# Optimization experiments

Hardware: AMD Instinct MI355X
Metric: run time of the kernel (lower is better)

Reference implementation:

```python
import jax, jax.numpy as jnp
import numpy as np

V, E = 50000, 800000
NODE_IN, EDGE_IN, OUT, HEADS = 128, 16, 32, 4
NEG_SLOPE = 0.2  # DGL EdgeGATConv default negative_slope


def setup_inputs() -> dict:
    key = jax.random.key(0)
    ks = jax.random.split(key, 10)
    return {
        "node_feats": jax.random.normal(ks[0], (V, NODE_IN), jnp.float32),
        "edge_feats": jax.random.normal(ks[1], (E, EDGE_IN), jnp.float32),
        "src": jax.random.randint(ks[2], (E,), 0, V),
        "dst": jax.random.randint(ks[3], (E,), 0, V),
        "W_node": jax.random.normal(ks[4], (NODE_IN, HEADS * OUT), jnp.float32) * 0.05,
        "W_edge": jax.random.normal(ks[5], (EDGE_IN, HEADS * OUT), jnp.float32) * 0.05,
        "attn_l": jax.random.normal(ks[6], (HEADS, OUT), jnp.float32) * 0.05,
        "attn_r": jax.random.normal(ks[7], (HEADS, OUT), jnp.float32) * 0.05,
        "attn_e": jax.random.normal(ks[8], (HEADS, OUT), jnp.float32) * 0.05,
        "res_W": jax.random.normal(ks[9], (NODE_IN, HEADS * OUT), jnp.float32) * 0.05,
        "bias": jnp.zeros((HEADS * OUT,), jnp.float32),
    }


def _leaky_relu(x, slope):
    return jnp.where(x >= 0, x, slope * x)


def reference(node_feats, edge_feats, src, dst, W_node, W_edge, attn_l, attn_r, attn_e, res_W, bias):
    V = node_feats.shape[0]
    H, F = attn_l.shape
    # linear projections
    ft = (node_feats @ W_node).reshape(V, H, F)    # [V,H,F]
    fe = (edge_feats @ W_edge).reshape(-1, H, F)   # [E,H,F]
    # per-head attention logits
    el = jnp.einsum('vhf,hf->vh', ft, attn_l)      # [V,H]
    er = jnp.einsum('vhf,hf->vh', ft, attn_r)      # [V,H]
    ee = jnp.einsum('ehf,hf->eh', fe, attn_e)      # [E,H]
    e = _leaky_relu(el[src] + er[dst] + ee, NEG_SLOPE)  # [E,H]
    # edge softmax over incoming edges of each destination node (stable)
    emax = jax.ops.segment_max(e, dst, num_segments=V)  # [V,H]
    ex = jnp.exp(e - emax[dst])
    esum = jax.ops.segment_sum(ex, dst, num_segments=V)  # [V,H]
    a = ex / esum[dst]                                   # [E,H]
    # weighted message passing: u_mul_e(ft, a) then sum to dst
    msg = ft[src] * a[:, :, None]                        # [E,H,F]
    rst = jax.ops.segment_sum(msg, dst, num_segments=V)  # [V,H,F]
    # residual connection + bias (EdgeGATConv residual=True, bias=True)
    rst = rst + (node_feats @ res_W).reshape(V, H, F)
    rst = rst + bias.reshape(1, H, F)
    # agg_mode='flatten': concat heads
    return rst.reshape(V, H * F)
```

## Files before the change

### kernel.cpp

```cpp
#include <hip/hip_runtime.h>
#include <hip/hip_fp16.h>
#include <cstdint>

#define V_N 50000
#define E_N 800000
#define NODE_IN 128
#define EDGE_IN 16
#define HF 128
#define NEG_SLOPE 0.2f
#define NB_SCAN 196
#define NODE_BLKS 1563
#define HIST_BLKS 3125

#define OFF_FT    0
#define OFF_EL    3200000
#define OFF_ER    3400000
#define OFF_DEG   3600000
#define OFF_ROW   3650000
#define OFF_BSUM  3700004
#define OFF_RANK  3700260
#define OFF_REC   4500260
#define OFF_WATT  7700260
#define OFF_BFRAG 7700324

typedef short bf16x8 __attribute__((ext_vector_type(8)));
typedef float f32x4 __attribute__((ext_vector_type(4)));

__device__ __forceinline__ unsigned short f2bf(float f) {
    unsigned u = __float_as_uint(f);
    u += 0x7fffu + ((u >> 16) & 1u);
    return (unsigned short)(u >> 16);
}
__device__ __forceinline__ unsigned pk2(float lo, float hi) {
    return (unsigned)f2bf(lo) | ((unsigned)f2bf(hi) << 16);
}
__device__ __forceinline__ float bflo(unsigned w) { return __uint_as_float(w << 16); }
__device__ __forceinline__ float bfhi(unsigned w) { return __uint_as_float(w & 0xffff0000u); }

typedef __fp16 fp16x2 __attribute__((ext_vector_type(2)));
__device__ __forceinline__ unsigned pkh2(float a, float b) {
    fp16x2 h = __builtin_amdgcn_cvt_pkrtz(a, b);
    return __builtin_bit_cast(unsigned, h);
}
__device__ __forceinline__ __half2 u2h(unsigned u) {
    return __builtin_bit_cast(__half2, u);
}
__device__ __forceinline__ unsigned h2u(__half2 h) {
    return __builtin_bit_cast(unsigned, h);
}

__global__ void k_prep(const float* __restrict__ We,
                       const float* __restrict__ attn_e,
                       const float* __restrict__ Wn,
                       const float* __restrict__ Wr,
                       float* __restrict__ watt,
                       unsigned* __restrict__ bfrag,
                       int* __restrict__ deg) {
    int g = blockIdx.x * 256 + threadIdx.x;
    for (int i = g; i < V_N; i += 16384) deg[i] = 0;
    if (blockIdx.x == 0 && threadIdx.x < 64) {
        int k = threadIdx.x >> 2, h = threadIdx.x & 3;
        float s = 0.f;
        #pragma unroll
        for (int f = 0; f < 32; f++)
            s += We[k * HF + h * 32 + f] * attn_e[h * 32 + f];
        watt[k * 4 + h] = s;
    }
    if (g < 16384) {
        int c    = g >> 8;
        int lane = (g >> 2) & 63;
        int jp   = g & 3;
        int nt = c >> 2, ks = c & 3;
        int col = nt * 16 + (lane & 15);
        int k   = ks * 32 + (lane >> 4) * 8 + jp * 2;
        const float* W = (col < 128) ? Wn : Wr;
        int cc = col & 127;
        float x0 = W[(size_t)k * 128 + cc];
        float x1 = W[(size_t)(k + 1) * 128 + cc];
        bfrag[g] = pk2(x0, x1);
    }
}

__global__ __launch_bounds__(256) void k_nodehist(
    const float* __restrict__ nf, const unsigned* __restrict__ bfragw,
    const float* __restrict__ attn_l, const float* __restrict__ attn_r,
    const float* __restrict__ bias, const int* __restrict__ dst,
    unsigned* __restrict__ ftw, float* __restrict__ el,
    float* __restrict__ er, float* __restrict__ out,
    int* __restrict__ deg, int* __restrict__ rank)
{
    __shared__ __align__(16) float sSf[32 * 140];
    unsigned short* sA = (unsigned short*)sSf;

    if (blockIdx.x >= NODE_BLKS) {
        int e = (blockIdx.x - NODE_BLKS) * 256 + threadIdx.x;
        rank[e] = atomicAdd(&deg[dst[e]], 1);
        return;
    }

    const int t = threadIdx.x;
    const int lane = t & 63;
    const int w = t >> 6;
    const int nb = blockIdx.x * 32;
    const int n15 = lane & 15;
    const int q = lane >> 4;
    const unsigned short* bfrag = (const unsigned short*)bfragw;

    #pragma unroll
    for (int i = 0; i < 4; i++) {
        int f = t + i * 256;
        int node = f >> 5;
        int kc = (f & 31) * 4;
        float4 v = {0.f, 0.f, 0.f, 0.f};
        if (nb + node < V_N)
            v = *(const float4*)(nf + (size_t)(nb + node) * NODE_IN + kc);
        uint2 u2 = make_uint2(pk2(v.x, v.y), pk2(v.z, v.w));
        *(uint2*)&sA[node * 136 + kc] = u2;
    }
    __syncthreads();

    f32x4 acc[2][4];
    #pragma unroll
    for (int m = 0; m < 2; m++)
        #pragma unroll
        for (int tt = 0; tt < 4; tt++) acc[m][tt] = (f32x4){0.f, 0.f, 0.f, 0.f};

    #pragma unroll
    for (int ks = 0; ks < 4; ks++) {
        bf16x8 a0 = *(const bf16x8*)&sA[n15 * 136 + ks * 32 + q * 8];
        bf16x8 a1 = *(const bf16x8*)&sA[(16 + n15) * 136 + ks * 32 + q * 8];
        #pragma unroll
        for (int tt = 0; tt < 4; tt++) {
            int nt = (tt < 2) ? (2 * w + tt) : (8 + 2 * w + (tt - 2));
            bf16x8 b = *(const bf16x8*)(bfrag + ((size_t)(nt * 4 + ks) * 64 + lane) * 8);
            acc[0][tt] = __builtin_amdgcn_mfma_f32_16x16x32_bf16(a0, b, acc[0][tt], 0, 0, 0);
            acc[1][tt] = __builtin_amdgcn_mfma_f32_16x16x32_bf16(a1, b, acc[1][tt], 0, 0, 0);
        }
    }

    {
        float al0 = attn_l[w * 32 + n15];
        float al1 = attn_l[w * 32 + 16 + n15];
        float ar0 = attn_r[w * 32 + n15];
        float ar1 = attn_r[w * 32 + 16 + n15];
        #pragma unroll
        for (int m = 0; m < 2; m++) {
            #pragma unroll
            for (int r = 0; r < 4; r++) {
                float fa = acc[m][0][r], fb = acc[m][1][r];
                float elp = fa * al0 + fb * al1;
                float erp = fa * ar0 + fb * ar1;
                elp += __shfl_xor(elp, 1); erp += __shfl_xor(erp, 1);
                elp += __shfl_xor(elp, 2); erp += __shfl_xor(erp, 2);
                elp += __shfl_xor(elp, 4); erp += __shfl_xor(erp, 4);
                elp += __shfl_xor(elp, 8); erp += __shfl_xor(erp, 8);
                int node = nb + m * 16 + q * 4 + r;
                if (n15 == 0 && node < V_N) {
                    el[node * 4 + w] = elp;
                    er[node * 4 + w] = erp;
                }
            }
        }
    }
    #pragma unroll
    for (int m = 0; m < 2; m++)
        #pragma unroll
        for (int r = 0; r < 4; r++) {
            int node = nb + m * 16 + q * 4 + r;
            if (node < V_N)
                ftw[(size_t)node * 64 + w * 16 + n15] =
                    pkh2(acc[m][0][r], acc[m][1][r]);
        }
    __syncthreads();

    #pragma unroll
    for (int m = 0; m < 2; m++)
        #pragma unroll
        for (int tt = 2; tt < 4; tt++)
            #pragma unroll
            for (int r = 0; r < 4; r++)
                sSf[(m * 16 + q * 4 + r) * 140 + w * 32 + (tt - 2) * 16 + n15] =
                    acc[m][tt][r];
    __syncthreads();
    #pragma unroll
    for (int i = 0; i < 4; i++) {
        int u = t + i * 256;
        int node = u >> 5, c4 = (u & 31) * 4;
        if (nb + node < V_N) {
            float4 v = *(float4*)&sSf[node * 140 + c4];
            float4 b4 = *(const float4*)(bias + c4);
            v.x += b4.x; v.y += b4.y; v.z += b4.z; v.w += b4.w;
            *(float4*)(out + (size_t)(nb + node) * HF + c4) = v;
        }
    }
}

__global__ __launch_bounds__(256) void k_scan(const int* __restrict__ deg,
                                              int* __restrict__ rowp) {
    __shared__ int sh[256];
    int t = threadIdx.x, b = blockIdx.x;

    int pre = 0;
    for (int i = t; i < b * 256; i += 256) pre += deg[i];
    sh[t] = pre;
    __syncthreads();
    #pragma unroll
    for (int off = 128; off > 0; off >>= 1) {
        if (t < off) sh[t] += sh[t + off];
        __syncthreads();
    }
    int sbase = sh[0];
    __syncthreads();

    int i = b * 256 + t;
    int v = (i < V_N) ? deg[i] : 0;
    sh[t] = v;
    __syncthreads();
    #pragma unroll
    for (int off = 1; off < 256; off <<= 1) {
        int u = (t >= off) ? sh[t - off] : 0;
        __syncthreads();
        sh[t] += u;
        __syncthreads();
    }
    if (i < V_N) rowp[i] = sbase + sh[t] - v;
    if (i == 0) rowp[V_N] = E_N;
}

__global__ __launch_bounds__(256) void k_escatter(
    const float* __restrict__ ef, const int* __restrict__ src,
    const int* __restrict__ dst, const int* __restrict__ rank,
    const int* __restrict__ rowp, const float* __restrict__ watt,
    const float* __restrict__ el, uint4* __restrict__ rec)
{
    __shared__ float sw[64];
    __shared__ __align__(16) float see[256][4];
    const int t = threadIdx.x;
    if (t < 64) sw[t] = watt[t];
    __syncthreads();
    const int base = blockIdx.x * 256;
    const int lane = t & 63, w = t >> 6;
    const int k0 = (lane & 3) * 4;

    #pragma unroll
    for (int r = 0; r < 4; r++) {
        int le = w * 64 + r * 16 + (lane >> 2);
        float4 v = *(const float4*)(ef + (size_t)(base + le) * EDGE_IN + k0);
        float e0 = 0.f, e1 = 0.f, e2 = 0.f, e3 = 0.f;
        float vv[4] = {v.x, v.y, v.z, v.w};
        #pragma unroll
        for (int j = 0; j < 4; j++) {
            int k = k0 + j;
            e0 += vv[j] * sw[k * 4 + 0];
            e1 += vv[j] * sw[k * 4 + 1];
            e2 += vv[j] * sw[k * 4 + 2];
            e3 += vv[j] * sw[k * 4 + 3];
        }
        e0 += __shfl_xor(e0, 1); e1 += __shfl_xor(e1, 1);
        e2 += __shfl_xor(e2, 1); e3 += __shfl_xor(e3, 1);
        e0 += __shfl_xor(e0, 2); e1 += __shfl_xor(e1, 2);
        e2 += __shfl_xor(e2, 2); e3 += __shfl_xor(e3, 2);
        if ((lane & 3) == 0) {
            float4 o = {e0, e1, e2, e3};
            *(float4*)&see[le][0] = o;
        }
    }
    __syncthreads();

    int e = base + t;
    int s = src[e], d = dst[e];
    int p = rowp[d] + rank[e];
    float4 ee = *(float4*)&see[t][0];
    float4 el4 = *(const float4*)(el + (size_t)s * 4);
    uint4 rr;
    rr.x = (unsigned)s;
    rr.y = pk2(el4.x + ee.x, el4.y + ee.y);
    rr.z = pk2(el4.z + ee.z, el4.w + ee.w);
    rr.w = 0;
    rec[p] = rr;
}

__global__ __launch_bounds__(256) void k_gather(
    const int* __restrict__ row, const uint4* __restrict__ rec,
    const float* __restrict__ er,
    const unsigned* __restrict__ ftw, float* __restrict__ out)
{
    __shared__ unsigned aw[4][64][4];
    const int lane = threadIdx.x & 63;
    const int wid  = threadIdx.x >> 6;
    const int d = blockIdx.x * 4 + wid;
    if (d >= V_N) return;
    const int n0 = row[d];
    const int deg = row[d + 1] - n0;
    if (deg == 0) return;

    const float4 er4 = *(const float4*)(er + (size_t)d * 4);

    const int qw = lane >> 4, li = lane & 15;
    const int head = li >> 2;
    float4 s4 = {0.f, 0.f, 0.f, 0.f};
    __half2 ha0 = u2h(0u), ha1 = u2h(0u), ha2 = u2h(0u), ha3 = u2h(0u);
    __half2 hb0 = u2h(0u), hb1 = u2h(0u), hb2 = u2h(0u), hb3 = u2h(0u);

    for (int i0 = 0; i0 < deg; i0 += 64) {
        int chunk = min(64, deg - i0);
        int si = 0;
        float4 ex = {0.f, 0.f, 0.f, 0.f};
        if (lane < chunk) {
            uint4 r = rec[n0 + i0 + lane];
            si = (int)r.x;
            float x0 = bflo(r.y) + er4.x;
            float x1 = bfhi(r.y) + er4.y;
            float x2 = bflo(r.z) + er4.z;
            float x3 = bfhi(r.z) + er4.w;
            x0 = x0 >= 0.f ? x0 : NEG_SLOPE * x0;
            x1 = x1 >= 0.f ? x1 : NEG_SLOPE * x1;
            x2 = x2 >= 0.f ? x2 : NEG_SLOPE * x2;
            x3 = x3 >= 0.f ? x3 : NEG_SLOPE * x3;
            ex.x = __expf(x0); ex.y = __expf(x1);
            ex.z = __expf(x2); ex.w = __expf(x3);
            s4.x += ex.x; s4.y += ex.y; s4.z += ex.z; s4.w += ex.w;
        }
        uint4 ap;
        ap.x = pkh2(ex.x, ex.x); ap.y = pkh2(ex.y, ex.y);
        ap.z = pkh2(ex.z, ex.z); ap.w = pkh2(ex.w, ex.w);
        *(uint4*)&aw[wid][lane][0] = ap;
        asm volatile("s_waitcnt lgkmcnt(0)" ::: "memory");

        int iters = (chunk + 7) & ~7;
        for (int j = 0; j < iters; j += 8) {
            int jq0 = j + qw, jq1 = j + qw + 4;
            int sidx0 = __shfl(si, jq0);
            int sidx1 = __shfl(si, jq1);
            unsigned au0 = aw[wid][jq0][head];
            unsigned au1 = aw[wid][jq1][head];
            uint4 wv0 = *(const uint4*)(ftw + (size_t)sidx0 * 64 + li * 4);
            uint4 wv1 = *(const uint4*)(ftw + (size_t)sidx1 * 64 + li * 4);
            ha0 = __hfma2(u2h(wv0.x), u2h(au0), ha0);
            ha1 = __hfma2(u2h(wv0.y), u2h(au0), ha1);
            ha2 = __hfma2(u2h(wv0.z), u2h(au0), ha2);
            ha3 = __hfma2(u2h(wv0.w), u2h(au0), ha3);
            hb0 = __hfma2(u2h(wv1.x), u2h(au1), hb0);
            hb1 = __hfma2(u2h(wv1.y), u2h(au1), hb1);
            hb2 = __hfma2(u2h(wv1.z), u2h(au1), hb2);
            hb3 = __hfma2(u2h(wv1.w), u2h(au1), hb3);
        }
    }
    #pragma unroll
    for (int off = 1; off < 64; off <<= 1) {
        s4.x += __shfl_xor(s4.x, off);
        s4.y += __shfl_xor(s4.y, off);
        s4.z += __shfl_xor(s4.z, off);
        s4.w += __shfl_xor(s4.w, off);
    }
    ha0 = __hadd2(ha0, hb0); ha1 = __hadd2(ha1, hb1);
    ha2 = __hadd2(ha2, hb2); ha3 = __hadd2(ha3, hb3);
    ha0 = __hadd2(ha0, u2h(__shfl_xor(h2u(ha0), 16)));
    ha1 = __hadd2(ha1, u2h(__shfl_xor(h2u(ha1), 16)));
    ha2 = __hadd2(ha2, u2h(__shfl_xor(h2u(ha2), 16)));
    ha3 = __hadd2(ha3, u2h(__shfl_xor(h2u(ha3), 16)));
    ha0 = __hadd2(ha0, u2h(__shfl_xor(h2u(ha0), 32)));
    ha1 = __hadd2(ha1, u2h(__shfl_xor(h2u(ha1), 32)));
    ha2 = __hadd2(ha2, u2h(__shfl_xor(h2u(ha2), 32)));
    ha3 = __hadd2(ha3, u2h(__shfl_xor(h2u(ha3), 32)));
    if (qw == 0) {
        float rsv = 1.f / (head == 0 ? s4.x : head == 1 ? s4.y :
                           head == 2 ? s4.z : s4.w);
        float* op = out + (size_t)d * HF + head * 32 + (li & 3) * 4;
        float4 r0 = *(float4*)op;
        r0.x += __low2float(ha0) * rsv; r0.y += __low2float(ha1) * rsv;
        r0.z += __low2float(ha2) * rsv; r0.w += __low2float(ha3) * rsv;
        *(float4*)op = r0;
        float4 r1 = *(float4*)(op + 16);
        r1.x += __high2float(ha0) * rsv; r1.y += __high2float(ha1) * rsv;
        r1.z += __high2float(ha2) * rsv; r1.w += __high2float(ha3) * rsv;
        *(float4*)(op + 16) = r1;
    }
}

extern "C" void kernel_launch(void* const* d_in, const int* in_sizes, int n_in,
                              void* d_out, int out_size, void* d_ws, size_t ws_size,
                              hipStream_t stream) {
    const float* nf     = (const float*)d_in[0];
    const float* ef     = (const float*)d_in[1];
    const int*   src    = (const int*)d_in[2];
    const int*   dst    = (const int*)d_in[3];
    const float* Wn     = (const float*)d_in[4];
    const float* We     = (const float*)d_in[5];
    const float* attn_l = (const float*)d_in[6];
    const float* attn_r = (const float*)d_in[7];
    const float* attn_e = (const float*)d_in[8];
    const float* Wr     = (const float*)d_in[9];
    const float* bias   = (const float*)d_in[10];
    float* out = (float*)d_out;

    unsigned* wsw  = (unsigned*)d_ws;
    unsigned* ftw  = wsw + OFF_FT;
    float* el      = (float*)(wsw + OFF_EL);
    float* er      = (float*)(wsw + OFF_ER);
    int* deg       = (int*)(wsw + OFF_DEG);
    int* rowp      = (int*)(wsw + OFF_ROW);
    int* rank      = (int*)(wsw + OFF_RANK);
    uint4* rec     = (uint4*)(wsw + OFF_REC);
    float* watt    = (float*)(wsw + OFF_WATT);
    unsigned* bfrag = wsw + OFF_BFRAG;

    k_prep<<<64, 256, 0, stream>>>(We, attn_e, Wn, Wr, watt, bfrag, deg);
    k_nodehist<<<NODE_BLKS + HIST_BLKS, 256, 0, stream>>>(
        nf, bfrag, attn_l, attn_r, bias, dst, ftw, el, er, out, deg, rank);
    k_scan<<<NB_SCAN, 256, 0, stream>>>(deg, rowp);
    k_escatter<<<E_N / 256, 256, 0, stream>>>(ef, src, dst, rank,
                                              rowp, watt, el, rec);
    k_gather<<<(V_N + 3) / 4, 256, 0, stream>>>(rowp, rec, er, ftw, out);
}
```

Before: 256.8 us.

## Regroup kernels: fuse histogram with prep, scan with node GEMM; 16-lane gather per node

The degree histogram now runs in the same launch as weight prep, and the prefix scan runs in the same launch as the node projection GEMM. This cuts one launch and overlaps the scan with GEMM work. The per-edge rank array is dropped: the scatter now claims slots with an atomic cursor per destination, which saves the rank write and read but makes ordering within a segment nondeterministic. The gather kernel maps 16 lanes to each destination node instead of a full 64-lane wavefront, which suits the low average degree but leaves fewer lanes for high-degree nodes.

```diff
diff --git a/kernel.cpp b/kernel.cpp
--- a/kernel.cpp
+++ b/kernel.cpp
@@ -11,14 +11,14 @@
 #define NB_SCAN 196
 #define NODE_BLKS 1563
 #define HIST_BLKS 3125
+#define PREP_BLKS 64
 
 #define OFF_FT    0
 #define OFF_EL    3200000
 #define OFF_ER    3400000
 #define OFF_DEG   3600000
 #define OFF_ROW   3650000
-#define OFF_BSUM  3700004
-#define OFF_RANK  3700260
+#define OFF_CUR   3700260
 #define OFF_REC   4500260
 #define OFF_WATT  7700260
 #define OFF_BFRAG 7700324
@@ -49,24 +49,29 @@
     return __builtin_bit_cast(unsigned, h);
 }
 
-__global__ void k_prep(const float* __restrict__ We,
-                       const float* __restrict__ attn_e,
-                       const float* __restrict__ Wn,
-                       const float* __restrict__ Wr,
-                       float* __restrict__ watt,
-                       unsigned* __restrict__ bfrag,
-                       int* __restrict__ deg) {
-    int g = blockIdx.x * 256 + threadIdx.x;
-    for (int i = g; i < V_N; i += 16384) deg[i] = 0;
-    if (blockIdx.x == 0 && threadIdx.x < 64) {
-        int k = threadIdx.x >> 2, h = threadIdx.x & 3;
+__global__ __launch_bounds__(256) void k_prephist(
+    const float* __restrict__ We, const float* __restrict__ attn_e,
+    const float* __restrict__ Wn, const float* __restrict__ Wr,
+    const int* __restrict__ dst,
+    float* __restrict__ watt, unsigned* __restrict__ bfrag,
+    int* __restrict__ deg)
+{
+    const int t = threadIdx.x;
+    if (blockIdx.x >= PREP_BLKS) {
+        int e = (blockIdx.x - PREP_BLKS) * 256 + t;
+        atomicAdd(&deg[dst[e]], 1);
+        return;
+    }
+    int g = blockIdx.x * 256 + t;
+    if (blockIdx.x == 0 && t < 64) {
+        int k = t >> 2, h = t & 3;
         float s = 0.f;
         #pragma unroll
         for (int f = 0; f < 32; f++)
             s += We[k * HF + h * 32 + f] * attn_e[h * 32 + f];
         watt[k * 4 + h] = s;
     }
-    if (g < 16384) {
+    {
         int c    = g >> 8;
         int lane = (g >> 2) & 63;
         int jp   = g & 3;
@@ -81,27 +86,55 @@
     }
 }
 
-__global__ __launch_bounds__(256) void k_nodehist(
+__global__ __launch_bounds__(256) void k_nodescan(
     const float* __restrict__ nf, const unsigned* __restrict__ bfragw,
     const float* __restrict__ attn_l, const float* __restrict__ attn_r,
-    const float* __restrict__ bias, const int* __restrict__ dst,
+    const float* __restrict__ bias, const int* __restrict__ deg,
     unsigned* __restrict__ ftw, float* __restrict__ el,
     float* __restrict__ er, float* __restrict__ out,
-    int* __restrict__ deg, int* __restrict__ rank)
+    int* __restrict__ rowp, int* __restrict__ cursor)
 {
     __shared__ __align__(16) float sSf[32 * 140];
     unsigned short* sA = (unsigned short*)sSf;
 
-    if (blockIdx.x >= NODE_BLKS) {
-        int e = (blockIdx.x - NODE_BLKS) * 256 + threadIdx.x;
-        rank[e] = atomicAdd(&deg[dst[e]], 1);
+    if (blockIdx.x < NB_SCAN) {
+        int* sh = (int*)sSf;
+        int t = threadIdx.x, b = blockIdx.x;
+        int pre = 0;
+        for (int i = t; i < b * 256; i += 256) pre += deg[i];
+        sh[t] = pre;
+        __syncthreads();
+        #pragma unroll
+        for (int off = 128; off > 0; off >>= 1) {
+            if (t < off) sh[t] += sh[t + off];
+            __syncthreads();
+        }
+        int sbase = sh[0];
+        __syncthreads();
+        int i = b * 256 + t;
+        int v = (i < V_N) ? deg[i] : 0;
+        sh[t] = v;
+        __syncthreads();
+        #pragma unroll
+        for (int off = 1; off < 256; off <<= 1) {
+            int u = (t >= off) ? sh[t - off] : 0;
+            __syncthreads();
+            sh[t] += u;
+            __syncthreads();
+        }
+        if (i < V_N) {
+            int r = sbase + sh[t] - v;
+            rowp[i] = r;
+            cursor[i] = r;
+        }
+        if (i == 0) rowp[V_N] = E_N;
         return;
     }
 
     const int t = threadIdx.x;
     const int lane = t & 63;
     const int w = t >> 6;
-    const int nb = blockIdx.x * 32;
+    const int nb = (blockIdx.x - NB_SCAN) * 32;
     const int n15 = lane & 15;
     const int q = lane >> 4;
     const unsigned short* bfrag = (const unsigned short*)bfragw;
@@ -195,43 +228,11 @@
     }
 }
 
-__global__ __launch_bounds__(256) void k_scan(const int* __restrict__ deg,
-                                              int* __restrict__ rowp) {
-    __shared__ int sh[256];
-    int t = threadIdx.x, b = blockIdx.x;
-
-    int pre = 0;
-    for (int i = t; i < b * 256; i += 256) pre += deg[i];
-    sh[t] = pre;
-    __syncthreads();
-    #pragma unroll
-    for (int off = 128; off > 0; off >>= 1) {
-        if (t < off) sh[t] += sh[t + off];
-        __syncthreads();
-    }
-    int sbase = sh[0];
-    __syncthreads();
-
-    int i = b * 256 + t;
-    int v = (i < V_N) ? deg[i] : 0;
-    sh[t] = v;
-    __syncthreads();
-    #pragma unroll
-    for (int off = 1; off < 256; off <<= 1) {
-        int u = (t >= off) ? sh[t - off] : 0;
-        __syncthreads();
-        sh[t] += u;
-        __syncthreads();
-    }
-    if (i < V_N) rowp[i] = sbase + sh[t] - v;
-    if (i == 0) rowp[V_N] = E_N;
-}
-
 __global__ __launch_bounds__(256) void k_escatter(
     const float* __restrict__ ef, const int* __restrict__ src,
-    const int* __restrict__ dst, const int* __restrict__ rank,
-    const int* __restrict__ rowp, const float* __restrict__ watt,
-    const float* __restrict__ el, uint4* __restrict__ rec)
+    const int* __restrict__ dst, int* __restrict__ cursor,
+    const float* __restrict__ watt, const float* __restrict__ el,
+    uint4* __restrict__ rec)
 {
     __shared__ float sw[64];
     __shared__ __align__(16) float see[256][4];
@@ -269,7 +270,7 @@
 
     int e = base + t;
     int s = src[e], d = dst[e];
-    int p = rowp[d] + rank[e];
+    int p = atomicAdd(&cursor[d], 1);
     float4 ee = *(float4*)&see[t][0];
     float4 el4 = *(const float4*)(el + (size_t)s * 4);
     uint4 rr;
@@ -285,29 +286,28 @@
     const float* __restrict__ er,
     const unsigned* __restrict__ ftw, float* __restrict__ out)
 {
-    __shared__ unsigned aw[4][64][4];
-    const int lane = threadIdx.x & 63;
-    const int wid  = threadIdx.x >> 6;
-    const int d = blockIdx.x * 4 + wid;
-    if (d >= V_N) return;
+    __shared__ unsigned aw[16][16][4];
+    const int t = threadIdx.x;
+    const int g = t >> 4;
+    const int li = t & 15;
+    const int head = li >> 2;
+    const int lanebase = t & 48;
+    const int d = blockIdx.x * 16 + g;
     const int n0 = row[d];
     const int deg = row[d + 1] - n0;
     if (deg == 0) return;
 
     const float4 er4 = *(const float4*)(er + (size_t)d * 4);
-
-    const int qw = lane >> 4, li = lane & 15;
-    const int head = li >> 2;
     float4 s4 = {0.f, 0.f, 0.f, 0.f};
     __half2 ha0 = u2h(0u), ha1 = u2h(0u), ha2 = u2h(0u), ha3 = u2h(0u);
     __half2 hb0 = u2h(0u), hb1 = u2h(0u), hb2 = u2h(0u), hb3 = u2h(0u);
 
-    for (int i0 = 0; i0 < deg; i0 += 64) {
-        int chunk = min(64, deg - i0);
+    for (int i0 = 0; i0 < deg; i0 += 16) {
+        int chunk = min(16, deg - i0);
         int si = 0;
         float4 ex = {0.f, 0.f, 0.f, 0.f};
-        if (lane < chunk) {
-            uint4 r = rec[n0 + i0 + lane];
+        if (li < chunk) {
+            uint4 r = rec[n0 + i0 + li];
             si = (int)r.x;
             float x0 = bflo(r.y) + er4.x;
             float x1 = bfhi(r.y) + er4.y;
@@ -324,30 +324,29 @@
         uint4 ap;
         ap.x = pkh2(ex.x, ex.x); ap.y = pkh2(ex.y, ex.y);
         ap.z = pkh2(ex.z, ex.z); ap.w = pkh2(ex.w, ex.w);
-        *(uint4*)&aw[wid][lane][0] = ap;
+        *(uint4*)&aw[g][li][0] = ap;
         asm volatile("s_waitcnt lgkmcnt(0)" ::: "memory");
 
-        int iters = (chunk + 7) & ~7;
-        for (int j = 0; j < iters; j += 8) {
-            int jq0 = j + qw, jq1 = j + qw + 4;
-            int sidx0 = __shfl(si, jq0);
-            int sidx1 = __shfl(si, jq1);
-            unsigned au0 = aw[wid][jq0][head];
-            unsigned au1 = aw[wid][jq1][head];
-            uint4 wv0 = *(const uint4*)(ftw + (size_t)sidx0 * 64 + li * 4);
-            uint4 wv1 = *(const uint4*)(ftw + (size_t)sidx1 * 64 + li * 4);
-            ha0 = __hfma2(u2h(wv0.x), u2h(au0), ha0);
-            ha1 = __hfma2(u2h(wv0.y), u2h(au0), ha1);
-            ha2 = __hfma2(u2h(wv0.z), u2h(au0), ha2);
-            ha3 = __hfma2(u2h(wv0.w), u2h(au0), ha3);
-            hb0 = __hfma2(u2h(wv1.x), u2h(au1), hb0);
-            hb1 = __hfma2(u2h(wv1.y), u2h(au1), hb1);
-            hb2 = __hfma2(u2h(wv1.z), u2h(au1), hb2);
-            hb3 = __hfma2(u2h(wv1.w), u2h(au1), hb3);
-        }
-    }
-    #pragma unroll
-    for (int off = 1; off < 64; off <<= 1) {
+        int ce = (chunk + 1) & ~1;
+        for (int j = 0; j < ce; j += 2) {
+            int s0 = __shfl(si, lanebase + j);
+            int s1 = __shfl(si, lanebase + j + 1);
+            unsigned a0 = aw[g][j][head];
+            unsigned a1 = aw[g][j + 1][head];
+            uint4 w0 = *(const uint4*)(ftw + (size_t)s0 * 64 + li * 4);
+            uint4 w1 = *(const uint4*)(ftw + (size_t)s1 * 64 + li * 4);
+            ha0 = __hfma2(u2h(w0.x), u2h(a0), ha0);
+            ha1 = __hfma2(u2h(w0.y), u2h(a0), ha1);
+            ha2 = __hfma2(u2h(w0.z), u2h(a0), ha2);
+            ha3 = __hfma2(u2h(w0.w), u2h(a0), ha3);
+            hb0 = __hfma2(u2h(w1.x), u2h(a1), hb0);
+            hb1 = __hfma2(u2h(w1.y), u2h(a1), hb1);
+            hb2 = __hfma2(u2h(w1.z), u2h(a1), hb2);
+            hb3 = __hfma2(u2h(w1.w), u2h(a1), hb3);
+        }
+    }
+    #pragma unroll
+    for (int off = 1; off < 16; off <<= 1) {
         s4.x += __shfl_xor(s4.x, off);
         s4.y += __shfl_xor(s4.y, off);
         s4.z += __shfl_xor(s4.z, off);
@@ -355,27 +354,18 @@
     }
     ha0 = __hadd2(ha0, hb0); ha1 = __hadd2(ha1, hb1);
     ha2 = __hadd2(ha2, hb2); ha3 = __hadd2(ha3, hb3);
-    ha0 = __hadd2(ha0, u2h(__shfl_xor(h2u(ha0), 16)));
-    ha1 = __hadd2(ha1, u2h(__shfl_xor(h2u(ha1), 16)));
-    ha2 = __hadd2(ha2, u2h(__shfl_xor(h2u(ha2), 16)));
-    ha3 = __hadd2(ha3, u2h(__shfl_xor(h2u(ha3), 16)));
-    ha0 = __hadd2(ha0, u2h(__shfl_xor(h2u(ha0), 32)));
-    ha1 = __hadd2(ha1, u2h(__shfl_xor(h2u(ha1), 32)));
-    ha2 = __hadd2(ha2, u2h(__shfl_xor(h2u(ha2), 32)));
-    ha3 = __hadd2(ha3, u2h(__shfl_xor(h2u(ha3), 32)));
-    if (qw == 0) {
-        float rsv = 1.f / (head == 0 ? s4.x : head == 1 ? s4.y :
-                           head == 2 ? s4.z : s4.w);
-        float* op = out + (size_t)d * HF + head * 32 + (li & 3) * 4;
-        float4 r0 = *(float4*)op;
-        r0.x += __low2float(ha0) * rsv; r0.y += __low2float(ha1) * rsv;
-        r0.z += __low2float(ha2) * rsv; r0.w += __low2float(ha3) * rsv;
-        *(float4*)op = r0;
-        float4 r1 = *(float4*)(op + 16);
-        r1.x += __high2float(ha0) * rsv; r1.y += __high2float(ha1) * rsv;
-        r1.z += __high2float(ha2) * rsv; r1.w += __high2float(ha3) * rsv;
-        *(float4*)(op + 16) = r1;
-    }
+
+    float rsv = 1.f / (head == 0 ? s4.x : head == 1 ? s4.y :
+                       head == 2 ? s4.z : s4.w);
+    float* op = out + (size_t)d * HF + head * 32 + (li & 3) * 4;
+    float4 r0 = *(float4*)op;
+    r0.x += __low2float(ha0) * rsv; r0.y += __low2float(ha1) * rsv;
+    r0.z += __low2float(ha2) * rsv; r0.w += __low2float(ha3) * rsv;
+    *(float4*)op = r0;
+    float4 r1 = *(float4*)(op + 16);
+    r1.x += __high2float(ha0) * rsv; r1.y += __high2float(ha1) * rsv;
+    r1.z += __high2float(ha2) * rsv; r1.w += __high2float(ha3) * rsv;
+    *(float4*)(op + 16) = r1;
 }
 
 extern "C" void kernel_launch(void* const* d_in, const int* in_sizes, int n_in,
@@ -400,16 +390,17 @@
     float* er      = (float*)(wsw + OFF_ER);
     int* deg       = (int*)(wsw + OFF_DEG);
     int* rowp      = (int*)(wsw + OFF_ROW);
-    int* rank      = (int*)(wsw + OFF_RANK);
+    int* cursor    = (int*)(wsw + OFF_CUR);
     uint4* rec     = (uint4*)(wsw + OFF_REC);
     float* watt    = (float*)(wsw + OFF_WATT);
     unsigned* bfrag = wsw + OFF_BFRAG;
 
-    k_prep<<<64, 256, 0, stream>>>(We, attn_e, Wn, Wr, watt, bfrag, deg);
-    k_nodehist<<<NODE_BLKS + HIST_BLKS, 256, 0, stream>>>(
-        nf, bfrag, attn_l, attn_r, bias, dst, ftw, el, er, out, deg, rank);
-    k_scan<<<NB_SCAN, 256, 0, stream>>>(deg, rowp);
-    k_escatter<<<E_N / 256, 256, 0, stream>>>(ef, src, dst, rank,
-                                              rowp, watt, el, rec);
-    k_gather<<<(V_N + 3) / 4, 256, 0, stream>>>(rowp, rec, er, ftw, out);
-}
+    hipMemsetAsync(deg, 0, V_N * sizeof(int), stream);
+    k_prephist<<<PREP_BLKS + HIST_BLKS, 256, 0, stream>>>(
+        We, attn_e, Wn, Wr, dst, watt, bfrag, deg);
+    k_nodescan<<<NB_SCAN + NODE_BLKS, 256, 0, stream>>>(
+        nf, bfrag, attn_l, attn_r, bias, deg, ftw, el, er, out, rowp, cursor);
+    k_escatter<<<E_N / 256, 256, 0, stream>>>(ef, src, dst, cursor,
+                                              watt, el, rec);
+    k_gather<<<V_N / 16, 256, 0, stream>>>(rowp, rec, er, ftw, out);
+}
```

New measurement: 263.8 us. +2.7%, slower.
